# Kernel tuning notes

Hardware: AMD Instinct MI355X
Metric: run time of the kernel (lower is better)

The kernel has to match this reference:

```python
import jax, jax.numpy as jnp
import numpy as np
from jax import lax

D_MODEL = 1024
D_IN = 1024        # expand=1 -> d_inner = d_model
N_STATE = 16       # d_state
DT_RANK = 64       # ceil(d_model/16)
D_FFN = 4096
BATCH, SEQ = 2, 2048


def setup_inputs() -> dict:
    key = jax.random.key(0)
    ks = jax.random.split(key, 12)
    r = lambda i, shape, s=0.02: jax.random.normal(ks[i], shape, jnp.float32) * s
    ones = lambda n: jnp.ones((n,), jnp.float32)
    zeros = lambda n: jnp.zeros((n,), jnp.float32)
    # S4D-real init for A
    A_log = jnp.log(jnp.tile(jnp.arange(1, N_STATE + 1, dtype=jnp.float32), (D_IN, 1)))
    return {
        "src": jax.random.normal(ks[0], (BATCH, SEQ, D_MODEL), jnp.float32),
        "in_proj_w": r(1, (2 * D_IN, D_MODEL)),
        "conv_w": r(2, (D_IN, 2), 0.5),
        "conv_b": zeros(D_IN),
        "x_proj_w": r(3, (DT_RANK + 2 * N_STATE, D_IN)),
        "dt_proj_w": r(4, (D_IN, DT_RANK), 0.1),
        "dt_proj_b": r(5, (D_IN,), 0.1),
        "A_log": A_log,
        "Dp": ones(D_IN),
        "out_proj_w": r(6, (D_MODEL, D_IN)),
        "mnorm_g": ones(D_MODEL), "mnorm_b": zeros(D_MODEL),
        "n1_g": ones(D_MODEL), "n1_b": zeros(D_MODEL),
        "n2_g": ones(D_MODEL), "n2_b": zeros(D_MODEL),
        "n3_g": ones(D_MODEL), "n3_b": zeros(D_MODEL),
        "ffn_w1": r(7, (D_FFN, D_MODEL)),
        "ffn_w2": r(8, (D_MODEL, D_FFN)),
        "fe_w": r(9, (D_MODEL, D_MODEL)),
        "fe_b": zeros(D_MODEL),
    }


def _ln(x, g, b, eps=1e-5):
    m = x.mean(-1, keepdims=True)
    v = ((x - m) ** 2).mean(-1, keepdims=True)
    return (x - m) / jnp.sqrt(v + eps) * g + b


def _mamba(x, in_proj_w, conv_w, conv_b, x_proj_w, dt_proj_w, dt_proj_b,
           A_log, Dp, out_proj_w):
    B, L, _ = x.shape
    xz = x @ in_proj_w.T                       # (B,L,2*D_IN)
    x_in, z = jnp.split(xz, 2, axis=-1)
    # depthwise causal conv1d, kernel size 2: y[l] = w0*x[l-1] + w1*x[l] + b
    x_prev = jnp.pad(x_in, ((0, 0), (1, 0), (0, 0)))[:, :L]
    x_c = jax.nn.silu(x_prev * conv_w[:, 0] + x_in * conv_w[:, 1] + conv_b)
    x_dbl = x_c @ x_proj_w.T                   # (B,L,DT_RANK+2N)
    dt, Bm, Cm = jnp.split(x_dbl, [DT_RANK, DT_RANK + N_STATE], axis=-1)
    delta = jax.nn.softplus(dt @ dt_proj_w.T + dt_proj_b)   # (B,L,D_IN)
    A = -jnp.exp(A_log)                        # (D_IN,N)
    deltaA = jnp.exp(delta[..., None] * A)                   # (B,L,D_IN,N)
    dBu = delta[..., None] * Bm[:, :, None, :] * x_c[..., None]

    def step(h, t):
        dA_t, dBu_t, C_t = t                   # (B,D_IN,N),(B,D_IN,N),(B,N)
        h = dA_t * h + dBu_t
        y = jnp.einsum('bdn,bn->bd', h, C_t)
        return h, y

    h0 = jnp.zeros((B, D_IN, N_STATE), x.dtype)
    _, ys = lax.scan(step, h0,
                     (deltaA.transpose(1, 0, 2, 3),
                      dBu.transpose(1, 0, 2, 3),
                      Cm.transpose(1, 0, 2)))
    y = ys.transpose(1, 0, 2)                  # (B,L,D_IN)
    y = (y + x_c * Dp) * jax.nn.silu(z)
    return y @ out_proj_w.T


def reference(src, in_proj_w, conv_w, conv_b, x_proj_w, dt_proj_w, dt_proj_b,
              A_log, Dp, out_proj_w, mnorm_g, mnorm_b, n1_g, n1_b, n2_g, n2_b,
              n3_g, n3_b, ffn_w1, ffn_w2, fe_w, fe_b):
    # src1 = MambaBlock(norm1(src)); dropout = identity (eval)
    h = _mamba(_ln(src, n1_g, n1_b), in_proj_w, conv_w, conv_b, x_proj_w,
               dt_proj_w, dt_proj_b, A_log, Dp, out_proj_w)
    src = src + _ln(h, mnorm_g, mnorm_b)
    # FFN: Linear -> LeakyReLU(0.01) -> Linear (no bias)
    f = _ln(src, n2_g, n2_b) @ ffn_w1.T
    f = jnp.where(f >= 0, f, 0.01 * f) @ ffn_w2.T
    src = src + f
    src = src + (_ln(src, n3_g, n3_b) @ fe_w.T + fe_b)
    return src
```

## Files before the change

kernel.cpp:

```cpp
#include <hip/hip_runtime.h>
#include <hip/hip_bf16.h>
#include <cstddef>

#define L_SEQ   2048
#define NBATCH  2
#define NROWS   (NBATCH * L_SEQ)
#define NSTATE  16
#define CH      64
#define NCHUNK  (L_SEQ / CH)

typedef __bf16 bf16x8 __attribute__((ext_vector_type(8)));
typedef float  f32x4  __attribute__((ext_vector_type(4)));
typedef unsigned short u16x4 __attribute__((ext_vector_type(4)));
typedef unsigned short u16x8 __attribute__((ext_vector_type(8)));

static __device__ __forceinline__ unsigned short f2bf(float f) {
  unsigned int x = __builtin_bit_cast(unsigned int, f);
  x += 0x7fffu + ((x >> 16) & 1u);
  return (unsigned short)(x >> 16);
}
static __device__ __forceinline__ float bf2f(unsigned short u) {
  return __builtin_bit_cast(float, ((unsigned int)u) << 16);
}

#define GLDS(g, l) __builtin_amdgcn_global_load_lds( \
    (const __attribute__((address_space(1))) void*)(g), \
    (__attribute__((address_space(3))) void*)(l), 16, 0, 0)

#define DRAIN_VM() asm volatile("s_waitcnt vmcnt(0)" ::: "memory")

__global__ __launch_bounds__(256) void cvt_bf16_kernel(
    const float* __restrict__ in, unsigned short* __restrict__ out, int n4)
{
  const int i = blockIdx.x * 256 + threadIdx.x;
  if (i < n4) {
    const float4 v = reinterpret_cast<const float4*>(in)[i];
    u16x4 o;
    o[0] = f2bf(v.x); o[1] = f2bf(v.y); o[2] = f2bf(v.z); o[3] = f2bf(v.w);
    reinterpret_cast<u16x4*>(out)[i] = o;
  }
}

__global__ __launch_bounds__(256) void cvt_all_kernel(
    const float* __restrict__ ipw, const float* __restrict__ xpw,
    const float* __restrict__ dtw, const float* __restrict__ opw,
    const float* __restrict__ w1,  const float* __restrict__ w2,
    const float* __restrict__ few, float* __restrict__ zx,
    unsigned short* __restrict__ o_ipw, unsigned short* __restrict__ o_xpw,
    unsigned short* __restrict__ o_dtw, unsigned short* __restrict__ o_opw,
    unsigned short* __restrict__ o_w1,  unsigned short* __restrict__ o_w2,
    unsigned short* __restrict__ o_few)
{
  int i = blockIdx.x * 256 + threadIdx.x;
  if (i < 98304) {
    reinterpret_cast<float4*>(zx)[i] = make_float4(0.f, 0.f, 0.f, 0.f);
    return;
  }
  i -= 98304;
  const float* src; unsigned short* dst;
  if (i < 524288)                 { src = ipw; dst = o_ipw; }
  else if ((i -= 524288) < 24576) { src = xpw; dst = o_xpw; }
  else if ((i -= 24576) < 16384)  { src = dtw; dst = o_dtw; }
  else if ((i -= 16384) < 262144) { src = opw; dst = o_opw; }
  else if ((i -= 262144) < 1048576){ src = w1; dst = o_w1; }
  else if ((i -= 1048576) < 1048576){ src = w2; dst = o_w2; }
  else if ((i -= 1048576) < 262144){ src = few; dst = o_few; }
  else return;
  const float4 v = reinterpret_cast<const float4*>(src)[i];
  u16x4 o;
  o[0] = f2bf(v.x); o[1] = f2bf(v.y); o[2] = f2bf(v.z); o[3] = f2bf(v.w);
  reinterpret_cast<u16x4*>(dst)[i] = o;
}

__global__ __launch_bounds__(256) void ln_kernel(
    const float* __restrict__ in, const float* __restrict__ g,
    const float* __restrict__ bta, const float* __restrict__ res,
    float* __restrict__ out, unsigned short* __restrict__ outb)
{
  const int row = blockIdx.x;
  const int tid = threadIdx.x;
  __shared__ float sm[8];
  const float4 v = reinterpret_cast<const float4*>(in + (size_t)row * 1024)[tid];
  float s = v.x + v.y + v.z + v.w;
#pragma unroll
  for (int o = 32; o > 0; o >>= 1) s += __shfl_down(s, o, 64);
  if ((tid & 63) == 0) sm[tid >> 6] = s;
  __syncthreads();
  const float mean = (sm[0] + sm[1] + sm[2] + sm[3]) * (1.f / 1024.f);
  const float dx = v.x - mean, dy = v.y - mean, dz = v.z - mean, dw = v.w - mean;
  float q = dx * dx + dy * dy + dz * dz + dw * dw;
#pragma unroll
  for (int o = 32; o > 0; o >>= 1) q += __shfl_down(q, o, 64);
  __syncthreads();
  if ((tid & 63) == 0) sm[tid >> 6] = q;
  __syncthreads();
  const float var = (sm[0] + sm[1] + sm[2] + sm[3]) * (1.f / 1024.f);
  const float rstd = rsqrtf(var + 1e-5f);
  const float4 gv = reinterpret_cast<const float4*>(g)[tid];
  const float4 bv = reinterpret_cast<const float4*>(bta)[tid];
  float4 o4;
  o4.x = dx * rstd * gv.x + bv.x;
  o4.y = dy * rstd * gv.y + bv.y;
  o4.z = dz * rstd * gv.z + bv.z;
  o4.w = dw * rstd * gv.w + bv.w;
  if (outb) {
    u16x4 ob;
    ob[0] = f2bf(o4.x); ob[1] = f2bf(o4.y); ob[2] = f2bf(o4.z); ob[3] = f2bf(o4.w);
    reinterpret_cast<u16x4*>(outb + (size_t)row * 1024)[tid] = ob;
  } else {
    if (res) {
      const float4 rv = reinterpret_cast<const float4*>(res + (size_t)row * 1024)[tid];
      o4.x += rv.x; o4.y += rv.y; o4.z += rv.z; o4.w += rv.w;
    }
    reinterpret_cast<float4*>(out + (size_t)row * 1024)[tid] = o4;
  }
}

__global__ __launch_bounds__(256) void ln2_kernel(
    const float* __restrict__ in, const float* __restrict__ g1,
    const float* __restrict__ b1, const float* __restrict__ res,
    const float* __restrict__ g2, const float* __restrict__ b2,
    float* __restrict__ out1, unsigned short* __restrict__ out2b)
{
  const int row = blockIdx.x;
  const int tid = threadIdx.x;
  __shared__ float sm[8];
  const float4 v = reinterpret_cast<const float4*>(in + (size_t)row * 1024)[tid];
  float s = v.x + v.y + v.z + v.w;
#pragma unroll
  for (int o = 32; o > 0; o >>= 1) s += __shfl_down(s, o, 64);
  if ((tid & 63) == 0) sm[tid >> 6] = s;
  __syncthreads();
  const float mean = (sm[0] + sm[1] + sm[2] + sm[3]) * (1.f / 1024.f);
  const float dx = v.x - mean, dy = v.y - mean, dz = v.z - mean, dw = v.w - mean;
  float q = dx * dx + dy * dy + dz * dz + dw * dw;
#pragma unroll
  for (int o = 32; o > 0; o >>= 1) q += __shfl_down(q, o, 64);
  __syncthreads();
  if ((tid & 63) == 0) sm[tid >> 6] = q;
  __syncthreads();
  const float var = (sm[0] + sm[1] + sm[2] + sm[3]) * (1.f / 1024.f);
  const float rstd = rsqrtf(var + 1e-5f);
  const float4 g1v = reinterpret_cast<const float4*>(g1)[tid];
  const float4 b1v = reinterpret_cast<const float4*>(b1)[tid];
  const float4 rv = reinterpret_cast<const float4*>(res + (size_t)row * 1024)[tid];
  float4 o4;
  o4.x = dx * rstd * g1v.x + b1v.x + rv.x;
  o4.y = dy * rstd * g1v.y + b1v.y + rv.y;
  o4.z = dz * rstd * g1v.z + b1v.z + rv.z;
  o4.w = dw * rstd * g1v.w + b1v.w + rv.w;
  reinterpret_cast<float4*>(out1 + (size_t)row * 1024)[tid] = o4;
  __syncthreads();
  float s2 = o4.x + o4.y + o4.z + o4.w;
#pragma unroll
  for (int o = 32; o > 0; o >>= 1) s2 += __shfl_down(s2, o, 64);
  if ((tid & 63) == 0) sm[tid >> 6] = s2;
  __syncthreads();
  const float mean2 = (sm[0] + sm[1] + sm[2] + sm[3]) * (1.f / 1024.f);
  const float ex = o4.x - mean2, ey = o4.y - mean2, ez = o4.z - mean2, ew = o4.w - mean2;
  float q2 = ex * ex + ey * ey + ez * ez + ew * ew;
#pragma unroll
  for (int o = 32; o > 0; o >>= 1) q2 += __shfl_down(q2, o, 64);
  __syncthreads();
  if ((tid & 63) == 0) sm[tid >> 6] = q2;
  __syncthreads();
  const float var2 = (sm[0] + sm[1] + sm[2] + sm[3]) * (1.f / 1024.f);
  const float rstd2 = rsqrtf(var2 + 1e-5f);
  const float4 g2v = reinterpret_cast<const float4*>(g2)[tid];
  const float4 b2v = reinterpret_cast<const float4*>(b2)[tid];
  u16x4 ob;
  ob[0] = f2bf(ex * rstd2 * g2v.x + b2v.x);
  ob[1] = f2bf(ey * rstd2 * g2v.y + b2v.y);
  ob[2] = f2bf(ez * rstd2 * g2v.z + b2v.z);
  ob[3] = f2bf(ew * rstd2 * g2v.w + b2v.w);
  reinterpret_cast<u16x4*>(out2b + (size_t)row * 1024)[tid] = ob;
}

__global__ __launch_bounds__(512) void gemm256_kernel(
    const unsigned short* __restrict__ A, int lda,
    const unsigned short* __restrict__ B, int ldb,
    void* __restrict__ Cv, int ldc,
    const float* __restrict__ bias, const float* __restrict__ res,
    int K, int act, int outbf, int gy)
{
  __shared__ __align__(16) unsigned char smem[131072];
  const int t = threadIdx.x;
  const int w = t >> 6, l = t & 63;

  const int q = gridDim.x >> 3;
  const int nid = (blockIdx.x & 7) * q + (blockIdx.x >> 3);
  const int bm = (nid / gy) * 256;
  const int bn = (nid % gy) * 256;

  const int wr = (w >> 2) * 128;
  const int wc = (w & 3) * 64;
  f32x4 acc[8][4] = {};

  const int srow = t >> 3;
  const int sk8 = (t & 7) * 8;
  const unsigned short* gA = A + (size_t)(bm + srow) * lda + sk8;
  const unsigned short* gB = B + (size_t)(bn + srow) * ldb + sk8;

  const int fr = l & 15;
  const int kb = (l >> 4) * 8;

#define SA6(buf) (smem + (buf) * 32768)
#define SB6(buf) (smem + 65536 + (buf) * 32768)

#define STAGE6(buf, k0) do { \
    _Pragma("unroll") \
    for (int ii = 0; ii < 4; ++ii) { \
      GLDS(gA + (k0) + (size_t)(ii * 64) * lda, SA6(buf) + ii * 8192 + w * 1024); \
      GLDS(gB + (k0) + (size_t)(ii * 64) * ldb, SB6(buf) + ii * 8192 + w * 1024); \
    } \
  } while (0)

#define COMPUTE6(buf) do { \
    _Pragma("unroll") \
    for (int s = 0; s < 2; ++s) { \
      bf16x8 af[8], bfr[4]; \
      _Pragma("unroll") \
      for (int j = 0; j < 4; ++j) \
        bfr[j] = *reinterpret_cast<const bf16x8*>((const unsigned short*)SB6(buf) + (wc + j * 16 + fr) * 64 + s * 32 + kb); \
      _Pragma("unroll") \
      for (int i = 0; i < 8; ++i) \
        af[i] = *reinterpret_cast<const bf16x8*>((const unsigned short*)SA6(buf) + (wr + i * 16 + fr) * 64 + s * 32 + kb); \
      _Pragma("unroll") \
      for (int i = 0; i < 8; ++i) \
        _Pragma("unroll") \
        for (int j = 0; j < 4; ++j) \
          acc[i][j] = __builtin_amdgcn_mfma_f32_16x16x32_bf16(af[i], bfr[j], acc[i][j], 0, 0, 0); \
    } \
  } while (0)

  STAGE6(0, 0);
  DRAIN_VM();
  __syncthreads();
  int cur = 0;
  for (int k0 = 64; k0 < K; k0 += 64) {
    __builtin_amdgcn_sched_barrier(0);
    STAGE6(cur ^ 1, k0);
    __builtin_amdgcn_sched_barrier(0);
    COMPUTE6(cur);
    DRAIN_VM();
    __syncthreads();
    cur ^= 1;
  }
  COMPUTE6(cur);
#undef STAGE6
#undef COMPUTE6
#undef SA6
#undef SB6

  const int crow = (l >> 4) * 4;
  const int ccol = l & 15;
  float* Cf = (float*)Cv;
  unsigned short* Cb = (unsigned short*)Cv;
#pragma unroll
  for (int i = 0; i < 8; ++i) {
#pragma unroll
    for (int j = 0; j < 4; ++j) {
      const int n = bn + wc + j * 16 + ccol;
      const float bv = bias ? bias[n] : 0.f;
#pragma unroll
      for (int r = 0; r < 4; ++r) {
        const int m = bm + wr + i * 16 + crow + r;
        float v = acc[i][j][r] + bv;
        if (act == 1) v = (v > 20.f) ? v : __logf(1.f + __expf(v));
        else if (act == 2) v = (v >= 0.f) ? v : 0.01f * v;
        if (res) v += res[(size_t)m * ldc + n];
        if (outbf) Cb[(size_t)m * ldc + n] = f2bf(v);
        else       Cf[(size_t)m * ldc + n] = v;
      }
    }
  }
}

template<int BK>
__global__ __launch_bounds__(512) void gemm_ksplit_kernel(
    const unsigned short* __restrict__ A, int lda,
    const unsigned short* __restrict__ B, int ldb,
    void* __restrict__ Cv, int ldc,
    const float* __restrict__ bias, const float* __restrict__ res,
    int K, int act, int outbf, int gy)
{
  constexpr int ABYTES = 128 * BK * 2;
  constexpr int NISS = (BK == 32) ? 2 : 4;
  constexpr int RPI  = (BK == 32) ? 64 : 32;
  constexpr int NS   = BK / 32;
  __shared__ __align__(16) unsigned char smem[8 * ABYTES];
  const int tid = threadIdx.x;
  const int grp = tid >> 8;
  const int t = tid & 255;
  const int w = t >> 6, l = t & 63;

  const int q = gridDim.x >> 3;
  const int nid = (blockIdx.x & 7) * q + (blockIdx.x >> 3);
  const int bm = (nid / gy) * 128;
  const int bn = (nid % gy) * 128;

  const int K2 = K >> 1;
  const int koff = grp * K2;
  const int wr = (w >> 1) * 64, wc = (w & 1) * 64;
  f32x4 acc[4][4] = {};

  const int srow = (BK == 32) ? (t >> 2) : (t >> 3);
  const int sk   = (BK == 32) ? ((t & 3) * 8) : ((t & 7) * 8);
  const unsigned short* gA = A + (size_t)(bm + srow) * lda + koff + sk;
  const unsigned short* gB = B + (size_t)(bn + srow) * ldb + koff + sk;

  const int gbase = grp * 2 * ABYTES;
  const int fr = l & 15;
  const int kb = (l >> 4) * 8;

#define SAb(buf) (smem + gbase + (buf) * ABYTES)
#define SBb(buf) (smem + 4 * ABYTES + gbase + (buf) * ABYTES)

#define STAGEK(buf, k0) do { \
    _Pragma("unroll") \
    for (int ii = 0; ii < NISS; ++ii) { \
      GLDS(gA + (k0) + (size_t)ii * RPI * lda, SAb(buf) + ii * 4096 + w * 1024); \
      GLDS(gB + (k0) + (size_t)ii * RPI * ldb, SBb(buf) + ii * 4096 + w * 1024); \
    } \
  } while (0)

#define COMPUTEK(buf) do { \
    _Pragma("unroll") \
    for (int s = 0; s < NS; ++s) { \
      bf16x8 af[4], bfr[4]; \
      _Pragma("unroll") \
      for (int i = 0; i < 4; ++i) \
        af[i] = *reinterpret_cast<const bf16x8*>((const unsigned short*)SAb(buf) + (wr + i * 16 + fr) * BK + s * 32 + kb); \
      _Pragma("unroll") \
      for (int j = 0; j < 4; ++j) \
        bfr[j] = *reinterpret_cast<const bf16x8*>((const unsigned short*)SBb(buf) + (wc + j * 16 + fr) * BK + s * 32 + kb); \
      _Pragma("unroll") \
      for (int i = 0; i < 4; ++i) \
        _Pragma("unroll") \
        for (int j = 0; j < 4; ++j) \
          acc[i][j] = __builtin_amdgcn_mfma_f32_16x16x32_bf16(af[i], bfr[j], acc[i][j], 0, 0, 0); \
    } \
  } while (0)

  STAGEK(0, 0);
  DRAIN_VM();
  __syncthreads();
  int cur = 0;
  for (int k0 = BK; k0 < K2; k0 += BK) {
    __builtin_amdgcn_sched_barrier(0);
    STAGEK(cur ^ 1, k0);
    __builtin_amdgcn_sched_barrier(0);
    COMPUTEK(cur);
    DRAIN_VM();
    __syncthreads();
    cur ^= 1;
  }
  COMPUTEK(cur);
#undef STAGEK
#undef COMPUTEK
#undef SAb
#undef SBb

  __syncthreads();
  float* red = (float*)smem;
  if (grp) {
#pragma unroll
    for (int i = 0; i < 4; ++i)
#pragma unroll
      for (int j = 0; j < 4; ++j)
        *reinterpret_cast<f32x4*>(&red[(t << 6) + (i * 4 + j) * 4]) = acc[i][j];
  }
  __syncthreads();
  if (!grp) {
    const int crow = (l >> 4) * 4;
    const int ccol = l & 15;
    float* Cf = (float*)Cv;
    unsigned short* Cb = (unsigned short*)Cv;
#pragma unroll
    for (int i = 0; i < 4; ++i) {
#pragma unroll
      for (int j = 0; j < 4; ++j) {
        const f32x4 o = *reinterpret_cast<const f32x4*>(&red[(t << 6) + (i * 4 + j) * 4]);
        const int n = bn + wc + j * 16 + ccol;
        const float bv = bias ? bias[n] : 0.f;
#pragma unroll
        for (int r = 0; r < 4; ++r) {
          const int m = bm + wr + i * 16 + crow + r;
          float v = acc[i][j][r] + o[r] + bv;
          if (act == 1) v = (v > 20.f) ? v : __logf(1.f + __expf(v));
          else if (act == 2) v = (v >= 0.f) ? v : 0.01f * v;
          if (res) v += res[(size_t)m * ldc + n];
          if (outbf) Cb[(size_t)m * ldc + n] = f2bf(v);
          else       Cf[(size_t)m * ldc + n] = v;
        }
      }
    }
  }
}

__global__ __launch_bounds__(256) void xproj_kernel(
    const unsigned short* __restrict__ A, int lda,
    const unsigned short* __restrict__ B, int ldb,
    float* __restrict__ C)
{
  __shared__ unsigned short As[2][128 * 32];
  __shared__ unsigned short Bs[2][96 * 32];
  const int t = threadIdx.x;
  const int w = t >> 6, l = t & 63;
  const int bm = blockIdx.x * 128;
  const int kbase = blockIdx.y * 128;

  f32x4 acc[2][6] = {};

  const int srow = t >> 2;
  const int sk = (t & 3) * 8;
  const unsigned short* gA0 = A + (size_t)(bm + srow) * lda + kbase + sk;
  const unsigned short* gA1 = gA0 + (size_t)64 * lda;
  const unsigned short* gB0 = B + (size_t)srow * ldb + kbase + sk;
  const unsigned short* gB1 = gB0 + (size_t)64 * ldb;

  const int fr = l & 15;
  const int kb = (l >> 4) * 8;

#define STAGEX(buf, k0) do { \
    GLDS(gA0 + (k0), &As[buf][w * 512]); \
    GLDS(gA1 + (k0), &As[buf][2048 + w * 512]); \
    GLDS(gB0 + (k0), &Bs[buf][w * 512]); \
    if (w < 2) GLDS(gB1 + (k0), &Bs[buf][2048 + w * 512]); \
  } while (0)

#define COMPUTEX(buf) do { \
    bf16x8 af[2], bfr[6]; \
    _Pragma("unroll") \
    for (int i = 0; i < 2; ++i) \
      af[i] = *reinterpret_cast<const bf16x8*>(&As[buf][(w * 32 + i * 16 + fr) * 32 + kb]); \
    _Pragma("unroll") \
    for (int j = 0; j < 6; ++j) \
      bfr[j] = *reinterpret_cast<const bf16x8*>(&Bs[buf][(j * 16 + fr) * 32 + kb]); \
    _Pragma("unroll") \
    for (int i = 0; i < 2; ++i) \
      _Pragma("unroll") \
      for (int j = 0; j < 6; ++j) \
        acc[i][j] = __builtin_amdgcn_mfma_f32_16x16x32_bf16(af[i], bfr[j], acc[i][j], 0, 0, 0); \
  } while (0)

  STAGEX(0, 0);
  DRAIN_VM();
  __syncthreads();
  int cur = 0;
  for (int s = 1; s < 4; ++s) {
    __builtin_amdgcn_sched_barrier(0);
    STAGEX(cur ^ 1, s * 32);
    __builtin_amdgcn_sched_barrier(0);
    COMPUTEX(cur);
    DRAIN_VM();
    __syncthreads();
    cur ^= 1;
  }
  COMPUTEX(cur);
#undef STAGEX
#undef COMPUTEX

  const int crow = (l >> 4) * 4;
  const int ccol = l & 15;
#pragma unroll
  for (int i = 0; i < 2; ++i)
#pragma unroll
    for (int j = 0; j < 6; ++j)
#pragma unroll
      for (int r = 0; r < 4; ++r) {
        const int m = bm + w * 32 + i * 16 + crow + r;
        const int n = j * 16 + ccol;
        atomicAdd(&C[(size_t)m * 96 + n], acc[i][j][r]);
      }
}

__global__ __launch_bounds__(256) void conv_silu_kernel(
    const unsigned short* __restrict__ xz, const float* __restrict__ cw,
    const float* __restrict__ cb, unsigned short* __restrict__ xcb)
{
  const int i = blockIdx.x * 256 + threadIdx.x;
  const int row = i >> 7;
  const int dv = (i & 127) * 8;
  const int l = row & (L_SEQ - 1);
  const u16x8 cur = *reinterpret_cast<const u16x8*>(&xz[(size_t)row * 2048 + dv]);
  u16x8 prev = {};
  if (l != 0) prev = *reinterpret_cast<const u16x8*>(&xz[(size_t)(row - 1) * 2048 + dv]);
  float cwv[16], cbv[8];
#pragma unroll
  for (int qq = 0; qq < 4; ++qq)
    *reinterpret_cast<float4*>(&cwv[qq * 4]) = reinterpret_cast<const float4*>(cw + 2 * dv)[qq];
#pragma unroll
  for (int qq = 0; qq < 2; ++qq)
    *reinterpret_cast<float4*>(&cbv[qq * 4]) = reinterpret_cast<const float4*>(cb + dv)[qq];
  u16x8 o;
#pragma unroll
  for (int e = 0; e < 8; ++e) {
    const float v = bf2f(prev[e]) * cwv[2 * e] + bf2f(cur[e]) * cwv[2 * e + 1] + cbv[e];
    o[e] = f2bf(v / (1.f + __expf(-v)));
  }
  *reinterpret_cast<u16x8*>(&xcb[(size_t)row * 1024 + dv]) = o;
}

__global__ __launch_bounds__(256) void scan_pass1(
    const unsigned short* __restrict__ delta, const unsigned short* __restrict__ xc,
    const float* __restrict__ xdbl, const float* __restrict__ A_log,
    float* __restrict__ hfin, float* __restrict__ pcum)
{
  const int tid = threadIdx.x;
  const int db = blockIdx.x & 3;
  const int c = (blockIdx.x >> 2) & (NCHUNK - 1);
  const int b = blockIdx.x >> 7;
  const int d = db * 256 + tid;
  __shared__ float Bsh[CH][16];
  {
    const int lr = tid >> 2, q = tid & 3;
    const float* p = xdbl + ((size_t)(b * L_SEQ + c * CH + lr) * 96) + 64 + q * 4;
    *reinterpret_cast<float4*>(&Bsh[lr][q * 4]) = *reinterpret_cast<const float4*>(p);
  }
  float a[NSTATE];
#pragma unroll
  for (int n = 0; n < NSTATE; ++n) a[n] = -__expf(A_log[d * 16 + n]);
  __syncthreads();
  float h[NSTATE], P[NSTATE];
#pragma unroll
  for (int n = 0; n < NSTATE; ++n) { h[n] = 0.f; P[n] = 1.f; }
  const size_t rowbase = (size_t)(b * L_SEQ + c * CH);
  for (int s = 0; s < CH; ++s) {
    const size_t row = rowbase + s;
    const float dl = bf2f(delta[row * 1024 + d]);
    const float xcv = bf2f(xc[row * 1024 + d]);
#pragma unroll
    for (int n = 0; n < NSTATE; ++n) {
      const float dA = __expf(dl * a[n]);
      h[n] = h[n] * dA + (dl * Bsh[s][n]) * xcv;
      P[n] *= dA;
    }
  }
  const size_t base = ((size_t)((b * NCHUNK + c) * 1024 + d)) * 16;
  float4* hp = reinterpret_cast<float4*>(hfin + base);
  float4* pp = reinterpret_cast<float4*>(pcum + base);
#pragma unroll
  for (int qq = 0; qq < 4; ++qq) {
    hp[qq] = make_float4(h[qq * 4], h[qq * 4 + 1], h[qq * 4 + 2], h[qq * 4 + 3]);
    pp[qq] = make_float4(P[qq * 4], P[qq * 4 + 1], P[qq * 4 + 2], P[qq * 4 + 3]);
  }
}

__global__ __launch_bounds__(256) void scan_pass2(
    const float* __restrict__ hfin, const float* __restrict__ pcum,
    float* __restrict__ hstart)
{
  const int t = blockIdx.x * 256 + threadIdx.x;
  const int b = t >> 14;
  const int dn = t & 16383;
  const size_t base = (size_t)b * NCHUNK * 16384 + dn;
  float h = 0.f;
  for (int c = 0; c < NCHUNK; ++c) {
    const size_t idx = base + (size_t)c * 16384;
    hstart[idx] = h;
    h = pcum[idx] * h + hfin[idx];
  }
}

__global__ __launch_bounds__(256) void scan_pass3(
    const unsigned short* __restrict__ delta, const unsigned short* __restrict__ xc,
    const float* __restrict__ xdbl, const float* __restrict__ A_log,
    const float* __restrict__ hstart, const float* __restrict__ Dp,
    const unsigned short* __restrict__ xz, unsigned short* __restrict__ yout)
{
  const int tid = threadIdx.x;
  const int db = blockIdx.x & 3;
  const int c = (blockIdx.x >> 2) & (NCHUNK - 1);
  const int b = blockIdx.x >> 7;
  const int d = db * 256 + tid;
  __shared__ float Bsh[CH][16];
  __shared__ float Csh[CH][16];
  {
    const int lr = tid >> 2, q = tid & 3;
    const float* p = xdbl + ((size_t)(b * L_SEQ + c * CH + lr) * 96);
    *reinterpret_cast<float4*>(&Bsh[lr][q * 4]) = *reinterpret_cast<const float4*>(p + 64 + q * 4);
    *reinterpret_cast<float4*>(&Csh[lr][q * 4]) = *reinterpret_cast<const float4*>(p + 80 + q * 4);
  }
  float a[NSTATE];
#pragma unroll
  for (int n = 0; n < NSTATE; ++n) a[n] = -__expf(A_log[d * 16 + n]);
  float h[NSTATE];
  {
    const size_t base = ((size_t)((b * NCHUNK + c) * 1024 + d)) * 16;
    const float4* hp = reinterpret_cast<const float4*>(hstart + base);
#pragma unroll
    for (int qq = 0; qq < 4; ++qq) {
      const float4 v = hp[qq];
      h[qq * 4] = v.x; h[qq * 4 + 1] = v.y; h[qq * 4 + 2] = v.z; h[qq * 4 + 3] = v.w;
    }
  }
  const float dpv = Dp[d];
  __syncthreads();
  const size_t rowbase = (size_t)(b * L_SEQ + c * CH);
  for (int s = 0; s < CH; ++s) {
    const size_t row = rowbase + s;
    const float dl = bf2f(delta[row * 1024 + d]);
    const float xcv = bf2f(xc[row * 1024 + d]);
    float y = 0.f;
#pragma unroll
    for (int n = 0; n < NSTATE; ++n) {
      const float dA = __expf(dl * a[n]);
      h[n] = h[n] * dA + (dl * Bsh[s][n]) * xcv;
      y += h[n] * Csh[s][n];
    }
    const float z = bf2f(xz[row * 2048 + 1024 + d]);
    const float sil = z / (1.f + __expf(-z));
    yout[row * 1024 + d] = f2bf((y + xcv * dpv) * sil);
  }
}

extern "C" void kernel_launch(void* const* d_in, const int* in_sizes, int n_in,
                              void* d_out, int out_size, void* d_ws, size_t ws_size,
                              hipStream_t stream)
{
  (void)in_sizes; (void)n_in; (void)out_size; (void)ws_size;
  const float* src        = (const float*)d_in[0];
  const float* in_proj_w  = (const float*)d_in[1];
  const float* conv_w     = (const float*)d_in[2];
  const float* conv_b     = (const float*)d_in[3];
  const float* x_proj_w   = (const float*)d_in[4];
  const float* dt_proj_w  = (const float*)d_in[5];
  const float* dt_proj_b  = (const float*)d_in[6];
  const float* A_log      = (const float*)d_in[7];
  const float* Dp         = (const float*)d_in[8];
  const float* out_proj_w = (const float*)d_in[9];
  const float* mnorm_g    = (const float*)d_in[10];
  const float* mnorm_b    = (const float*)d_in[11];
  const float* n1_g       = (const float*)d_in[12];
  const float* n1_b       = (const float*)d_in[13];
  const float* n2_g       = (const float*)d_in[14];
  const float* n2_b       = (const float*)d_in[15];
  const float* n3_g       = (const float*)d_in[16];
  const float* n3_b       = (const float*)d_in[17];
  const float* ffn_w1     = (const float*)d_in[18];
  const float* ffn_w2     = (const float*)d_in[19];
  const float* fe_w       = (const float*)d_in[20];
  const float* fe_b       = (const float*)d_in[21];
  float* out = (float*)d_out;
  float* ws  = (float*)d_ws;

  unsigned short* xzb   = (unsigned short*)ws;
  unsigned short* xdblb = (unsigned short*)(ws + 4194304);
  unsigned short* dtwb  = (unsigned short*)(ws + 4390912);
  unsigned short* deltab= (unsigned short*)(ws + 4423680);
  float* xdbl  = ws + 12582912;
  float* s5    = ws + 17301504;
  float* src1  = ws + 21495808;
  float* hfin  = ws + 25690112;
  float* pcum  = ws + 26738688;
  float* hst   = ws + 27787264;
  unsigned short* s1b  = (unsigned short*)(ws + 28835840);
  unsigned short* xcb  = (unsigned short*)(ws + 30932992);
  unsigned short* yb   = (unsigned short*)(ws + 33030144);
  unsigned short* f1b  = (unsigned short*)(ws + 35127296);
  unsigned short* ipwb = (unsigned short*)(ws + 43515904);
  unsigned short* xpwb = (unsigned short*)(ws + 44564480);
  unsigned short* opwb = (unsigned short*)(ws + 44613632);
  unsigned short* w1b  = (unsigned short*)(ws + 45137920);
  unsigned short* w2b  = (unsigned short*)(ws + 47235072);
  unsigned short* fewb = (unsigned short*)(ws + 49332224);

  const dim3 blk(256);
  const dim3 blk512(512);

  cvt_all_kernel<<<12832, blk, 0, stream>>>(
      in_proj_w, x_proj_w, dt_proj_w, out_proj_w, ffn_w1, ffn_w2, fe_w, xdbl,
      ipwb, xpwb, dtwb, opwb, w1b, w2b, fewb);

  ln_kernel<<<NROWS, blk, 0, stream>>>(src, n1_g, n1_b, nullptr, nullptr, s1b);
  gemm_ksplit_kernel<32><<<512, blk512, 0, stream>>>(s1b, 1024, ipwb, 1024, xzb, 2048,
                                                     nullptr, nullptr, 1024, 0, 1, 16);
  conv_silu_kernel<<<2048, blk, 0, stream>>>(xzb, conv_w, conv_b, xcb);
  xproj_kernel<<<dim3(32, 8), blk, 0, stream>>>(xcb, 1024, xpwb, 1024, xdbl);
  cvt_bf16_kernel<<<384, blk, 0, stream>>>(xdbl, xdblb, 98304);
  gemm_ksplit_kernel<32><<<256, blk512, 0, stream>>>(xdblb, 96, dtwb, 64, deltab, 1024,
                                                     dt_proj_b, nullptr, 64, 1, 1, 8);
  scan_pass1<<<256, blk, 0, stream>>>(deltab, xcb, xdbl, A_log, hfin, pcum);
  scan_pass2<<<128, blk, 0, stream>>>(hfin, pcum, hst);
  scan_pass3<<<256, blk, 0, stream>>>(deltab, xcb, xdbl, A_log, hst, Dp, xzb, yb);
  gemm_ksplit_kernel<64><<<256, blk512, 0, stream>>>(yb, 1024, opwb, 1024, s5, 1024,
                                                     nullptr, nullptr, 1024, 0, 0, 8);
  ln2_kernel<<<NROWS, blk, 0, stream>>>(s5, mnorm_g, mnorm_b, src,
                                        n2_g, n2_b, src1, s1b);
  gemm256_kernel<<<256, blk512, 0, stream>>>(s1b, 1024, w1b, 1024, f1b, 4096,
                                             nullptr, nullptr, 1024, 2, 1, 16);
  gemm_ksplit_kernel<64><<<256, blk512, 0, stream>>>(f1b, 4096, w2b, 4096, s5, 1024,
                                                     nullptr, src1, 4096, 0, 0, 8);
  ln_kernel<<<NROWS, blk, 0, stream>>>(s5, n3_g, n3_b, nullptr, nullptr, s1b);
  gemm_ksplit_kernel<64><<<256, blk512, 0, stream>>>(s1b, 1024, fewb, 1024, out, 1024,
                                                     fe_b, s5, 1024, 0, 0, 8);
}
```

Measured before the change: 380.9 us.

## Fuse first LayerNorm into weight-conversion kernel and store scan carries in bf16

```diff
diff --git a/kernel.cpp b/kernel.cpp
--- a/kernel.cpp
+++ b/kernel.cpp
@@ -49,8 +49,40 @@
     unsigned short* __restrict__ o_ipw, unsigned short* __restrict__ o_xpw,
     unsigned short* __restrict__ o_dtw, unsigned short* __restrict__ o_opw,
     unsigned short* __restrict__ o_w1,  unsigned short* __restrict__ o_w2,
-    unsigned short* __restrict__ o_few)
-{
+    unsigned short* __restrict__ o_few,
+    const float* __restrict__ lsrc, const float* __restrict__ lg,
+    const float* __restrict__ lb, unsigned short* __restrict__ louth)
+{
+  __shared__ float sm[8];
+  if (blockIdx.x >= 12832) {
+    const int row = blockIdx.x - 12832;
+    const int tid = threadIdx.x;
+    const float4 v = reinterpret_cast<const float4*>(lsrc + (size_t)row * 1024)[tid];
+    float s = v.x + v.y + v.z + v.w;
+#pragma unroll
+    for (int o = 32; o > 0; o >>= 1) s += __shfl_down(s, o, 64);
+    if ((tid & 63) == 0) sm[tid >> 6] = s;
+    __syncthreads();
+    const float mean = (sm[0] + sm[1] + sm[2] + sm[3]) * (1.f / 1024.f);
+    const float dx = v.x - mean, dy = v.y - mean, dz = v.z - mean, dw = v.w - mean;
+    float q = dx * dx + dy * dy + dz * dz + dw * dw;
+#pragma unroll
+    for (int o = 32; o > 0; o >>= 1) q += __shfl_down(q, o, 64);
+    __syncthreads();
+    if ((tid & 63) == 0) sm[tid >> 6] = q;
+    __syncthreads();
+    const float var = (sm[0] + sm[1] + sm[2] + sm[3]) * (1.f / 1024.f);
+    const float rstd = rsqrtf(var + 1e-5f);
+    const float4 gv = reinterpret_cast<const float4*>(lg)[tid];
+    const float4 bv = reinterpret_cast<const float4*>(lb)[tid];
+    u16x4 ob;
+    ob[0] = f2bf(dx * rstd * gv.x + bv.x);
+    ob[1] = f2bf(dy * rstd * gv.y + bv.y);
+    ob[2] = f2bf(dz * rstd * gv.z + bv.z);
+    ob[3] = f2bf(dw * rstd * gv.w + bv.w);
+    reinterpret_cast<u16x4*>(louth + (size_t)row * 1024)[tid] = ob;
+    return;
+  }
   int i = blockIdx.x * 256 + threadIdx.x;
   if (i < 98304) {
     reinterpret_cast<float4*>(zx)[i] = make_float4(0.f, 0.f, 0.f, 0.f);
@@ -505,7 +537,7 @@
 __global__ __launch_bounds__(256) void scan_pass1(
     const unsigned short* __restrict__ delta, const unsigned short* __restrict__ xc,
     const float* __restrict__ xdbl, const float* __restrict__ A_log,
-    float* __restrict__ hfin, float* __restrict__ pcum)
+    unsigned short* __restrict__ hfin, unsigned short* __restrict__ pcum)
 {
   const int tid = threadIdx.x;
   const int db = blockIdx.x & 3;
@@ -538,18 +570,21 @@
     }
   }
   const size_t base = ((size_t)((b * NCHUNK + c) * 1024 + d)) * 16;
-  float4* hp = reinterpret_cast<float4*>(hfin + base);
-  float4* pp = reinterpret_cast<float4*>(pcum + base);
-#pragma unroll
-  for (int qq = 0; qq < 4; ++qq) {
-    hp[qq] = make_float4(h[qq * 4], h[qq * 4 + 1], h[qq * 4 + 2], h[qq * 4 + 3]);
-    pp[qq] = make_float4(P[qq * 4], P[qq * 4 + 1], P[qq * 4 + 2], P[qq * 4 + 3]);
-  }
+  u16x8 h0, h1, p0, p1;
+#pragma unroll
+  for (int n = 0; n < 8; ++n) {
+    h0[n] = f2bf(h[n]);     h1[n] = f2bf(h[n + 8]);
+    p0[n] = f2bf(P[n]);     p1[n] = f2bf(P[n + 8]);
+  }
+  *reinterpret_cast<u16x8*>(hfin + base) = h0;
+  *reinterpret_cast<u16x8*>(hfin + base + 8) = h1;
+  *reinterpret_cast<u16x8*>(pcum + base) = p0;
+  *reinterpret_cast<u16x8*>(pcum + base + 8) = p1;
 }
 
 __global__ __launch_bounds__(256) void scan_pass2(
-    const float* __restrict__ hfin, const float* __restrict__ pcum,
-    float* __restrict__ hstart)
+    const unsigned short* __restrict__ hfin, const unsigned short* __restrict__ pcum,
+    unsigned short* __restrict__ hstart)
 {
   const int t = blockIdx.x * 256 + threadIdx.x;
   const int b = t >> 14;
@@ -558,15 +593,15 @@
   float h = 0.f;
   for (int c = 0; c < NCHUNK; ++c) {
     const size_t idx = base + (size_t)c * 16384;
-    hstart[idx] = h;
-    h = pcum[idx] * h + hfin[idx];
+    hstart[idx] = f2bf(h);
+    h = bf2f(pcum[idx]) * h + bf2f(hfin[idx]);
   }
 }
 
 __global__ __launch_bounds__(256) void scan_pass3(
     const unsigned short* __restrict__ delta, const unsigned short* __restrict__ xc,
     const float* __restrict__ xdbl, const float* __restrict__ A_log,
-    const float* __restrict__ hstart, const float* __restrict__ Dp,
+    const unsigned short* __restrict__ hstart, const float* __restrict__ Dp,
     const unsigned short* __restrict__ xz, unsigned short* __restrict__ yout)
 {
   const int tid = threadIdx.x;
@@ -588,12 +623,10 @@
   float h[NSTATE];
   {
     const size_t base = ((size_t)((b * NCHUNK + c) * 1024 + d)) * 16;
-    const float4* hp = reinterpret_cast<const float4*>(hstart + base);
-#pragma unroll
-    for (int qq = 0; qq < 4; ++qq) {
-      const float4 v = hp[qq];
-      h[qq * 4] = v.x; h[qq * 4 + 1] = v.y; h[qq * 4 + 2] = v.z; h[qq * 4 + 3] = v.w;
-    }
+    const u16x8 v0 = *reinterpret_cast<const u16x8*>(hstart + base);
+    const u16x8 v1 = *reinterpret_cast<const u16x8*>(hstart + base + 8);
+#pragma unroll
+    for (int n = 0; n < 8; ++n) { h[n] = bf2f(v0[n]); h[n + 8] = bf2f(v1[n]); }
   }
   const float dpv = Dp[d];
   __syncthreads();
@@ -652,9 +685,9 @@
   float* xdbl  = ws + 12582912;
   float* s5    = ws + 17301504;
   float* src1  = ws + 21495808;
-  float* hfin  = ws + 25690112;
-  float* pcum  = ws + 26738688;
-  float* hst   = ws + 27787264;
+  unsigned short* hfin = (unsigned short*)(ws + 25690112);
+  unsigned short* pcum = (unsigned short*)(ws + 26738688);
+  unsigned short* hst  = (unsigned short*)(ws + 27787264);
   unsigned short* s1b  = (unsigned short*)(ws + 28835840);
   unsigned short* xcb  = (unsigned short*)(ws + 30932992);
   unsigned short* yb   = (unsigned short*)(ws + 33030144);
@@ -669,11 +702,11 @@
   const dim3 blk(256);
   const dim3 blk512(512);
 
-  cvt_all_kernel<<<12832, blk, 0, stream>>>(
+  cvt_all_kernel<<<16928, blk, 0, stream>>>(
       in_proj_w, x_proj_w, dt_proj_w, out_proj_w, ffn_w1, ffn_w2, fe_w, xdbl,
-      ipwb, xpwb, dtwb, opwb, w1b, w2b, fewb);
-
-  ln_kernel<<<NROWS, blk, 0, stream>>>(src, n1_g, n1_b, nullptr, nullptr, s1b);
+      ipwb, xpwb, dtwb, opwb, w1b, w2b, fewb,
+      src, n1_g, n1_b, s1b);
+
   gemm_ksplit_kernel<32><<<512, blk512, 0, stream>>>(s1b, 1024, ipwb, 1024, xzb, 2048,
                                                      nullptr, nullptr, 1024, 0, 1, 16);
   conv_silu_kernel<<<2048, blk, 0, stream>>>(xzb, conv_w, conv_b, xcb);
```

After: 378.4 us. No clear change (-0.7%).
